# Performance work log

Measured on AMD Instinct MI355X. Metric: run time of the kernel, lower is better.

The kernel has to match this reference:

```python
import jax, jax.numpy as jnp
import numpy as np
import math

B, S, H = 2, 2048, 2048
NH, LD = 16, 512
HD = H // NH


def setup_inputs() -> dict:
    key = jax.random.key(0)
    ks = jax.random.split(key, 9)
    sc = 0.02
    return {
        "x": jax.random.normal(ks[0], (B, S, H), dtype=jnp.float32),
        "wq": jax.random.normal(ks[1], (H, H), dtype=jnp.float32) * sc,
        "bq": jnp.zeros((H,), dtype=jnp.float32),
        "wk_lat": jax.random.normal(ks[2], (H, LD), dtype=jnp.float32) * sc,
        "wv_lat": jax.random.normal(ks[3], (H, LD), dtype=jnp.float32) * sc,
        "wk": jax.random.normal(ks[4], (LD, H), dtype=jnp.float32) * sc,
        "wv": jax.random.normal(ks[5], (LD, H), dtype=jnp.float32) * sc,
        "wo": jax.random.normal(ks[6], (H, H), dtype=jnp.float32) * sc,
        "bo": jnp.zeros((H,), dtype=jnp.float32),
    }


def reference(x, wq, bq, wk_lat, wv_lat, wk, wv, wo, bo):
    b, s, _ = x.shape
    # projections
    q = (x @ wq + bq).reshape(b, s, NH, HD).transpose(0, 2, 1, 3)  # [B,NH,S,HD]
    k_lat = x @ wk_lat  # [B,S,LD]
    v_lat = x @ wv_lat
    k = (k_lat @ wk).reshape(b, s, NH, HD).transpose(0, 2, 1, 3)
    v = (v_lat @ wv).reshape(b, s, NH, HD).transpose(0, 2, 1, 3)
    # causal attention
    scores = jnp.einsum('bhqd,bhkd->bhqk', q, k) / math.sqrt(HD)
    mask = jnp.tril(jnp.ones((s, s), dtype=bool))  # True = keep
    scores = jnp.where(mask, scores, -jnp.inf)
    weights = jax.nn.softmax(scores, axis=-1)
    out = jnp.einsum('bhqk,bhkd->bhqd', weights, v)
    out = out.transpose(0, 2, 1, 3).reshape(b, s, H)
    return out @ wo + bo
```

## Files before the change

kernel.cpp:

```cpp
#include <hip/hip_runtime.h>
#include <hip/hip_bf16.h>

#define PB   2
#define PS   2048
#define PH   2048
#define PNH  16
#define PLD  512
#define PHD  128
#define PM   (PB * PS)
#define PNCAT 3072
#define ATT_SCALE 0.08838834764831845f
#define ATT_MOFF 4.0f
#define ATT_SC2  0.12751744f
#define ATT_MO2  5.77078016f

typedef __attribute__((ext_vector_type(8))) short bf16x8;
typedef __attribute__((ext_vector_type(4))) float f32x4;

__device__ __forceinline__ unsigned short f2bf(float f) {
    unsigned int u = __float_as_uint(f);
    u += 0x7FFFu + ((u >> 16) & 1u);
    return (unsigned short)(u >> 16);
}

__device__ __forceinline__ void gl_lds16(const unsigned short* g, unsigned short* l) {
    __builtin_amdgcn_global_load_lds(
        (const __attribute__((address_space(1))) unsigned int*)g,
        (__attribute__((address_space(3))) unsigned int*)l, 16, 0, 0);
}

#define VMCNT(n)     asm volatile("s_waitcnt vmcnt(" #n ")" ::: "memory")
#define MEMFENCE()   asm volatile("" ::: "memory")

__global__ __launch_bounds__(256) void cast_f32_bf16_kernel(
    const float* __restrict__ in, unsigned short* __restrict__ out, int n)
{
    int i = (blockIdx.x * 256 + threadIdx.x) * 4;
    if (i >= n) return;
    float4 f = *(const float4*)(in + i);
    unsigned int a = (unsigned int)f2bf(f.x) | ((unsigned int)f2bf(f.y) << 16);
    unsigned int b = (unsigned int)f2bf(f.z) | ((unsigned int)f2bf(f.w) << 16);
    *(uint2*)(out + i) = make_uint2(a, b);
}

struct TC6 {
    const float* src[6];
    unsigned short* dst[6];
    int R[6];
    int C[6];
};

__global__ __launch_bounds__(256) void transpose_cast6_kernel(TC6 p)
{
    __shared__ float tile[32][33];
    const int z = blockIdx.z;
    const int r0 = blockIdx.y * 32, c0 = blockIdx.x * 32;
    const int R = p.R[z], C = p.C[z];
    if (r0 >= R || c0 >= C) return;
    const float* in = p.src[z];
    unsigned short* out = p.dst[z];
    int tx = threadIdx.x, ty = threadIdx.y;
#pragma unroll
    for (int i = 0; i < 32; i += 8)
        tile[ty + i][tx] = in[(size_t)(r0 + ty + i) * C + (c0 + tx)];
    __syncthreads();
#pragma unroll
    for (int i = 0; i < 32; i += 8)
        out[(size_t)(c0 + ty + i) * R + (r0 + tx)] = f2bf(tile[tx][ty + i]);
}

template<int EPI, bool HAS_BIAS>
__global__ __launch_bounds__(256, 3) void gemm97_kernel(
    const unsigned short* __restrict__ A, int lda,
    const unsigned short* __restrict__ BT,
    const float* __restrict__ bias, int nbias,
    void* __restrict__ Cout, int ldc, int K)
{
    __shared__ __align__(16) unsigned short As[128 * 64];
    __shared__ __align__(16) unsigned short Bs[128 * 64];

    const int tid  = threadIdx.x;
    const int wave = tid >> 6, lane = tid & 63;
    const int wm = wave >> 1, wn = wave & 1;
    const int quad = lane >> 4, l15 = lane & 15;
    const int sw = l15 & 7;

    const int gx  = gridDim.x;
    const int nwg = gx * gridDim.y;
    int wg = blockIdx.y * gx + blockIdx.x;
    if (!(nwg & 7)) wg = (wg & 7) * (nwg >> 3) + (wg >> 3);
    const int bm = (wg / gx) * 128, bn = (wg % gx) * 128;

    const int nt = K >> 6;

    const int srow = tid >> 3;
    const int scol = ((tid & 7) ^ (srow & 7)) << 3;
    const unsigned short* Ag = A  + (size_t)(bm + srow) * lda + scol;
    const unsigned short* Bg = BT + (size_t)(bn + srow) * K   + scol;
    unsigned short* const ldsA = &As[wave * 512];
    unsigned short* const ldsB = &Bs[wave * 512];

    auto ldA = [&](int m, int ks) -> bf16x8 {
        int ra = wm * 64 + m * 16 + l15;
        return *(const bf16x8*)&As[ra * 64 + (((ks * 4 + quad) ^ sw) << 3)];
    };
    auto ldB = [&](int j, int ks) -> bf16x8 {
        int rb = wn * 64 + j * 16 + l15;
        return *(const bf16x8*)&Bs[rb * 64 + (((ks * 4 + quad) ^ sw) << 3)];
    };

    f32x4 acc[4][4] = {};

    for (int kt = 0; kt < nt; ++kt) {
        const int k0 = kt * 64;
#pragma unroll
        for (int s = 0; s < 4; ++s) {
            gl_lds16(Ag + (size_t)(s * 32) * lda + k0, ldsA + s * 2048);
            gl_lds16(Bg + (size_t)(s * 32) * K   + k0, ldsB + s * 2048);
        }
        VMCNT(0);
        __syncthreads();

        bf16x8 bfr[4][2];
#pragma unroll
        for (int j = 0; j < 4; ++j)
#pragma unroll
            for (int ks = 0; ks < 2; ++ks) bfr[j][ks] = ldB(j, ks);
#pragma unroll
        for (int m = 0; m < 4; ++m) {
            bf16x8 a0 = ldA(m, 0), a1 = ldA(m, 1);
#pragma unroll
            for (int j = 0; j < 4; ++j) {
                acc[m][j] = __builtin_amdgcn_mfma_f32_16x16x32_bf16(a0, bfr[j][0], acc[m][j], 0, 0, 0);
                acc[m][j] = __builtin_amdgcn_mfma_f32_16x16x32_bf16(a1, bfr[j][1], acc[m][j], 0, 0, 0);
            }
        }
        __syncthreads();
    }

#pragma unroll
    for (int m = 0; m < 4; ++m)
#pragma unroll
        for (int j = 0; j < 4; ++j)
#pragma unroll
            for (int r = 0; r < 4; ++r) {
                int row = bm + wm * 64 + m * 16 + quad * 4 + r;
                int col = bn + wn * 64 + j * 16 + l15;
                float val = acc[m][j][r];
                if (HAS_BIAS && col < nbias) val += bias[col];
                if (EPI == 2) {
                    int bb = row >> 11, s = row & 2047, hh = col >> 7, d = col & 127;
                    size_t idx = ((size_t)((bb << 4) + hh) << 18) + ((size_t)(s >> 6) << 13)
                               + ((d >> 3) << 9) + ((s & 63) << 3) + (d & 7);
                    ((unsigned short*)Cout)[idx] = f2bf(val);
                } else if (EPI == 3) {
                    int bb = row >> 11, s = row & 2047, hh = col >> 7, d = col & 127;
                    size_t idx = ((size_t)((bb << 4) + hh) << 18) + ((size_t)(s >> 6) << 13)
                               + (((s >> 3) & 7) << 10) + (d << 3) + (s & 7);
                    ((unsigned short*)Cout)[idx] = f2bf(val);
                } else if (EPI == 1) {
                    ((float*)Cout)[(size_t)row * ldc + col] = val;
                } else {
                    ((unsigned short*)Cout)[(size_t)row * ldc + col] = f2bf(val);
                }
            }
}

__global__ __launch_bounds__(256, 3) void flash_attn_mfma_kernel(
    const unsigned short* __restrict__ q,
    const unsigned short* __restrict__ kswz,
    const unsigned short* __restrict__ vswz,
    unsigned short* __restrict__ o)
{
    __shared__ __align__(16) unsigned short Kl[8192];
    __shared__ __align__(16) unsigned short Vl[8192];
    __shared__ __align__(16) unsigned short Ps[4][16][76];

    const int tid  = threadIdx.x;
    const int wave = tid >> 6;
    const int lane = tid & 63;
    const int quad = lane >> 4, l15 = lane & 15;

    const int bid = blockIdx.x;
    const int qt = 31 - (bid >> 5);
    const int bh = bid & 31;
    const int b  = bh >> 4, h = bh & 15;
    const int q0 = qt * 64;

    const unsigned short* qbase = q + (size_t)(b * PS + q0) * PNCAT + h * PHD;
    const unsigned short* kbase = kswz + ((size_t)bh << 18);
    const unsigned short* vbase = vswz + ((size_t)bh << 18);

    auto stageK = [&](int it) {
        const unsigned short* kt = kbase + ((size_t)it << 13);
#pragma unroll
        for (int j = 0; j < 4; ++j)
            gl_lds16(kt + (wave * 4 + j) * 512 + lane * 8, &Kl[(wave * 4 + j) * 512]);
    };
    auto stageV = [&](int it) {
        const unsigned short* vt = vbase + ((size_t)it << 13);
#pragma unroll
        for (int j = 0; j < 4; ++j)
            gl_lds16(vt + (wave * 4 + j) * 512 + lane * 8, &Vl[(wave * 4 + j) * 512]);
    };

    bf16x8 aq[4];
#pragma unroll
    for (int kk = 0; kk < 4; ++kk)
        aq[kk] = *(const bf16x8*)(qbase + (size_t)(wave * 16 + l15) * PNCAT + kk * 32 + quad * 8);

    bf16x8 vones;
#pragma unroll
    for (int j = 0; j < 8; ++j) vones[j] = (short)0x3F80;

    f32x4 oacc[8] = {};
    f32x4 lacc = {};

    for (int it = 0; it <= qt; ++it) {
        __syncthreads();
        stageK(it);
        stageV(it);
        VMCNT(4);
        __builtin_amdgcn_s_barrier();
        MEMFENCE();

        f32x4 sacc[4] = {};
#pragma unroll
        for (int kk = 0; kk < 4; ++kk)
#pragma unroll
            for (int n = 0; n < 4; ++n) {
                bf16x8 bk = *(const bf16x8*)&Kl[((kk * 4 + quad) * 64 + n * 16 + l15) * 8];
                sacc[n] = __builtin_amdgcn_mfma_f32_16x16x32_bf16(aq[kk], bk, sacc[n], 0, 0, 0);
            }

        const bool diag = (it == qt);
#pragma unroll
        for (int n = 0; n < 4; ++n)
#pragma unroll
            for (int r = 0; r < 4; ++r) {
                float p = exp2f(fmaf(sacc[n][r], ATT_SC2, -ATT_MO2));
                if (diag && (n * 16 + l15 > wave * 16 + quad * 4 + r)) p = 0.0f;
                Ps[wave][quad * 4 + r][n * 16 + l15] = f2bf(p);
            }

        __syncthreads();

#pragma unroll
        for (int kk = 0; kk < 2; ++kk) {
            bf16x8 ap = *(const bf16x8*)&Ps[wave][l15][kk * 32 + quad * 8];
            lacc = __builtin_amdgcn_mfma_f32_16x16x32_bf16(ap, vones, lacc, 0, 0, 0);
#pragma unroll
            for (int n = 0; n < 8; ++n) {
                bf16x8 bv = *(const bf16x8*)&Vl[((kk * 4 + quad) * 128 + n * 16 + l15) * 8];
                oacc[n] = __builtin_amdgcn_mfma_f32_16x16x32_bf16(ap, bv, oacc[n], 0, 0, 0);
            }
        }
    }

    float inv[4];
#pragma unroll
    for (int r = 0; r < 4; ++r) inv[r] = 1.0f / lacc[r];
#pragma unroll
    for (int n = 0; n < 8; ++n)
#pragma unroll
        for (int r = 0; r < 4; ++r) {
            int row = q0 + wave * 16 + quad * 4 + r;
            int col = h * PHD + n * 16 + l15;
            o[(size_t)(b * PS + row) * PH + col] = f2bf(oacc[n][r] * inv[r]);
        }
}

extern "C" void kernel_launch(void* const* d_in, const int* in_sizes, int n_in,
                              void* d_out, int out_size, void* d_ws, size_t ws_size,
                              hipStream_t stream)
{
    const float* x      = (const float*)d_in[0];
    const float* wq     = (const float*)d_in[1];
    const float* bq     = (const float*)d_in[2];
    const float* wk_lat = (const float*)d_in[3];
    const float* wv_lat = (const float*)d_in[4];
    const float* wk     = (const float*)d_in[5];
    const float* wv     = (const float*)d_in[6];
    const float* wo     = (const float*)d_in[7];
    const float* bo     = (const float*)d_in[8];
    float* out = (float*)d_out;

    char* ws = (char*)d_ws;
    size_t off = 0;
    auto alloc = [&](size_t bytes) -> void* {
        void* p = ws + off;
        off += (bytes + 255) & ~(size_t)255;
        return p;
    };
    unsigned short* xb    = (unsigned short*)alloc((size_t)PM * PH * 2);
    unsigned short* wcatT = (unsigned short*)alloc((size_t)PNCAT * PH * 2);
    unsigned short* wkT   = (unsigned short*)alloc((size_t)PH * PLD * 2);
    unsigned short* wvT   = (unsigned short*)alloc((size_t)PH * PLD * 2);
    unsigned short* woT   = (unsigned short*)alloc((size_t)PH * PH * 2);
    unsigned short* cat   = (unsigned short*)alloc((size_t)PM * PNCAT * 2);
    unsigned short* kswz  = (unsigned short*)alloc((size_t)PM * PH * 2);
    unsigned short* attn  = (unsigned short*)alloc((size_t)PM * PH * 2);
    unsigned short* vswz  = xb;

    unsigned short* wqT    = wcatT;
    unsigned short* wkLatT = wcatT + (size_t)PH * PH;
    unsigned short* wvLatT = wcatT + (size_t)(PH + PLD) * PH;

    cast_f32_bf16_kernel<<<(PM * PH) / 4 / 256, 256, 0, stream>>>(x, xb, PM * PH);

    TC6 tc;
    tc.src[0] = wq;     tc.dst[0] = wqT;    tc.R[0] = PH;  tc.C[0] = PH;
    tc.src[1] = wk_lat; tc.dst[1] = wkLatT; tc.R[1] = PH;  tc.C[1] = PLD;
    tc.src[2] = wv_lat; tc.dst[2] = wvLatT; tc.R[2] = PH;  tc.C[2] = PLD;
    tc.src[3] = wk;     tc.dst[3] = wkT;    tc.R[3] = PLD; tc.C[3] = PH;
    tc.src[4] = wv;     tc.dst[4] = wvT;    tc.R[4] = PLD; tc.C[4] = PH;
    tc.src[5] = wo;     tc.dst[5] = woT;    tc.R[5] = PH;  tc.C[5] = PH;
    transpose_cast6_kernel<<<dim3(64, 64, 6), dim3(32, 8), 0, stream>>>(tc);

    gemm97_kernel<0, true><<<dim3(PNCAT / 128, PM / 128), 256, 0, stream>>>(
        xb, PH, wcatT, bq, PH, cat, PNCAT, PH);

    gemm97_kernel<2, false><<<dim3(PH / 128, PM / 128), 256, 0, stream>>>(
        cat + PH, PNCAT, wkT, nullptr, 0, kswz, 0, PLD);
    gemm97_kernel<3, false><<<dim3(PH / 128, PM / 128), 256, 0, stream>>>(
        cat + PH + PLD, PNCAT, wvT, nullptr, 0, vswz, 0, PLD);

    flash_attn_mfma_kernel<<<PB * PNH * (PS / 64), 256, 0, stream>>>(cat, kswz, vswz, attn);

    gemm97_kernel<1, true><<<dim3(PH / 128, PM / 128), 256, 0, stream>>>(
        attn, PH, woT, bo, PH, out, PH, PH);
}
```

Measured before the change: 337.1 us.

## Rewrite flash attention with 32x32 MFMA, 128-row query tiles and S^T formulation

The attention kernel now processes 128 query rows per block (32 per wave) instead of 64, switching from 16x16x32 to 32x32x16 bf16 MFMA and computing S^T = K·Q so each lane owns one query row. Row sums are accumulated in registers instead of through an extra ones-MFMA, and P is packed with v_cvt_pk_bf16. The K swizzle layout in the GEMM epilogue changes to match the new fragment reads. Halving the grid roughly doubles the K/V reuse per block, but it leaves fewer blocks and a coarser causal tail, and it raises register pressure from the 16-wide accumulators.

```diff
diff --git a/kernel.cpp b/kernel.cpp
--- a/kernel.cpp
+++ b/kernel.cpp
@@ -16,6 +16,7 @@
 
 typedef __attribute__((ext_vector_type(8))) short bf16x8;
 typedef __attribute__((ext_vector_type(4))) float f32x4;
+typedef __attribute__((ext_vector_type(16))) float f32x16;
 
 __device__ __forceinline__ unsigned short f2bf(float f) {
     unsigned int u = __float_as_uint(f);
@@ -31,6 +32,12 @@
 
 #define VMCNT(n)     asm volatile("s_waitcnt vmcnt(" #n ")" ::: "memory")
 #define MEMFENCE()   asm volatile("" ::: "memory")
+
+__device__ __forceinline__ unsigned int cvtpk_bf16(float lo, float hi) {
+    unsigned int r;
+    asm("v_cvt_pk_bf16_f32 %0, %1, %2" : "=v"(r) : "v"(lo), "v"(hi));
+    return r;
+}
 
 __global__ __launch_bounds__(256) void cast_f32_bf16_kernel(
     const float* __restrict__ in, unsigned short* __restrict__ out, int n)
@@ -151,7 +158,7 @@
                 if (EPI == 2) {
                     int bb = row >> 11, s = row & 2047, hh = col >> 7, d = col & 127;
                     size_t idx = ((size_t)((bb << 4) + hh) << 18) + ((size_t)(s >> 6) << 13)
-                               + ((d >> 3) << 9) + ((s & 63) << 3) + (d & 7);
+                               + ((d >> 4) << 10) + (((d >> 3) & 1) << 9) + ((s & 63) << 3) + (d & 7);
                     ((unsigned short*)Cout)[idx] = f2bf(val);
                 } else if (EPI == 3) {
                     int bb = row >> 11, s = row & 2047, hh = col >> 7, d = col & 127;
@@ -174,20 +181,21 @@
 {
     __shared__ __align__(16) unsigned short Kl[8192];
     __shared__ __align__(16) unsigned short Vl[8192];
-    __shared__ __align__(16) unsigned short Ps[4][16][76];
+    __shared__ __align__(16) unsigned short Pl[4][32][68];
 
     const int tid  = threadIdx.x;
     const int wave = tid >> 6;
     const int lane = tid & 63;
-    const int quad = lane >> 4, l15 = lane & 15;
+    const int l31 = lane & 31, hf = lane >> 5;
 
     const int bid = blockIdx.x;
-    const int qt = 31 - (bid >> 5);
+    const int qt = 15 - (bid >> 5);
     const int bh = bid & 31;
     const int b  = bh >> 4, h = bh & 15;
-    const int q0 = qt * 64;
-
-    const unsigned short* qbase = q + (size_t)(b * PS + q0) * PNCAT + h * PHD;
+    const int q0 = qt * 128;
+    const int nt = 2 * (qt + 1);
+
+    const unsigned short* qbase = q + (size_t)(b * PS + q0 + wave * 32 + l31) * PNCAT + h * PHD;
     const unsigned short* kbase = kswz + ((size_t)bh << 18);
     const unsigned short* vbase = vswz + ((size_t)bh << 18);
 
@@ -204,19 +212,16 @@
             gl_lds16(vt + (wave * 4 + j) * 512 + lane * 8, &Vl[(wave * 4 + j) * 512]);
     };
 
-    bf16x8 aq[4];
-#pragma unroll
-    for (int kk = 0; kk < 4; ++kk)
-        aq[kk] = *(const bf16x8*)(qbase + (size_t)(wave * 16 + l15) * PNCAT + kk * 32 + quad * 8);
-
-    bf16x8 vones;
-#pragma unroll
-    for (int j = 0; j < 8; ++j) vones[j] = (short)0x3F80;
-
-    f32x4 oacc[8] = {};
-    f32x4 lacc = {};
-
-    for (int it = 0; it <= qt; ++it) {
+    bf16x8 qf[8];
+#pragma unroll
+    for (int kk = 0; kk < 8; ++kk)
+        qf[kk] = *(const bf16x8*)(qbase + kk * 16 + hf * 8);
+
+    const int qrow = q0 + wave * 32 + l31;
+    f32x16 oacc[4] = {};
+    float lsum = 0.0f;
+
+    for (int it = 0; it < nt; ++it) {
         __syncthreads();
         stageK(it);
         stageV(it);
@@ -224,50 +229,63 @@
         __builtin_amdgcn_s_barrier();
         MEMFENCE();
 
-        f32x4 sacc[4] = {};
-#pragma unroll
-        for (int kk = 0; kk < 4; ++kk)
-#pragma unroll
-            for (int n = 0; n < 4; ++n) {
-                bf16x8 bk = *(const bf16x8*)&Kl[((kk * 4 + quad) * 64 + n * 16 + l15) * 8];
-                sacc[n] = __builtin_amdgcn_mfma_f32_16x16x32_bf16(aq[kk], bk, sacc[n], 0, 0, 0);
-            }
-
-        const bool diag = (it == qt);
-#pragma unroll
-        for (int n = 0; n < 4; ++n)
-#pragma unroll
-            for (int r = 0; r < 4; ++r) {
-                float p = exp2f(fmaf(sacc[n][r], ATT_SC2, -ATT_MO2));
-                if (diag && (n * 16 + l15 > wave * 16 + quad * 4 + r)) p = 0.0f;
-                Ps[wave][quad * 4 + r][n * 16 + l15] = f2bf(p);
-            }
+#pragma unroll
+        for (int m32 = 0; m32 < 2; ++m32) {
+            f32x16 s = {};
+#pragma unroll
+            for (int kk = 0; kk < 8; ++kk) {
+                bf16x8 ak = *(const bf16x8*)&Kl[(((kk * 2 + hf) * 64) + m32 * 32 + l31) * 8];
+                s = __builtin_amdgcn_mfma_f32_32x32x16_bf16(ak, qf[kk], s, 0, 0, 0);
+            }
+            const int kbase0 = it * 64 + m32 * 32 + 4 * hf;
+            const bool needmask = (it * 64 + m32 * 32 + 31) > (q0 + wave * 32);
+#pragma unroll
+            for (int r = 0; r < 16; r += 2) {
+                float p0 = exp2f(fmaf(s[r],     ATT_SC2, -ATT_MO2));
+                float p1 = exp2f(fmaf(s[r + 1], ATT_SC2, -ATT_MO2));
+                if (needmask) {
+                    int key = kbase0 + (r & 3) + 8 * (r >> 2);
+                    p0 = (key     <= qrow) ? p0 : 0.0f;
+                    p1 = (key + 1 <= qrow) ? p1 : 0.0f;
+                }
+                lsum += p0 + p1;
+                *(unsigned int*)&Pl[wave][l31][m32 * 32 + 4 * hf + 8 * (r >> 2) + (r & 3)]
+                    = cvtpk_bf16(p0, p1);
+            }
+        }
+
+        bf16x8 pa[4];
+#pragma unroll
+        for (int ks = 0; ks < 4; ++ks) {
+            uint2 w0 = *(const uint2*)&Pl[wave][l31][ks * 16 + hf * 8];
+            uint2 w1 = *(const uint2*)&Pl[wave][l31][ks * 16 + hf * 8 + 4];
+            uint4 w = {w0.x, w0.y, w1.x, w1.y};
+            pa[ks] = *(bf16x8*)&w;
+        }
 
         __syncthreads();
 
 #pragma unroll
-        for (int kk = 0; kk < 2; ++kk) {
-            bf16x8 ap = *(const bf16x8*)&Ps[wave][l15][kk * 32 + quad * 8];
-            lacc = __builtin_amdgcn_mfma_f32_16x16x32_bf16(ap, vones, lacc, 0, 0, 0);
-#pragma unroll
-            for (int n = 0; n < 8; ++n) {
-                bf16x8 bv = *(const bf16x8*)&Vl[((kk * 4 + quad) * 128 + n * 16 + l15) * 8];
-                oacc[n] = __builtin_amdgcn_mfma_f32_16x16x32_bf16(ap, bv, oacc[n], 0, 0, 0);
-            }
-        }
+        for (int ks = 0; ks < 4; ++ks)
+#pragma unroll
+            for (int dg = 0; dg < 4; ++dg) {
+                bf16x8 bv = *(const bf16x8*)&Vl[(((ks * 2 + hf) * 128) + dg * 32 + l31) * 8];
+                oacc[dg] = __builtin_amdgcn_mfma_f32_32x32x16_bf16(pa[ks], bv, oacc[dg], 0, 0, 0);
+            }
     }
 
-    float inv[4];
-#pragma unroll
-    for (int r = 0; r < 4; ++r) inv[r] = 1.0f / lacc[r];
-#pragma unroll
-    for (int n = 0; n < 8; ++n)
-#pragma unroll
-        for (int r = 0; r < 4; ++r) {
-            int row = q0 + wave * 16 + quad * 4 + r;
-            int col = h * PHD + n * 16 + l15;
-            o[(size_t)(b * PS + row) * PH + col] = f2bf(oacc[n][r] * inv[r]);
-        }
+    const float ltot = lsum + __shfl_xor(lsum, 32);
+    const float inv = 1.0f / ltot;
+
+#pragma unroll
+    for (int r = 0; r < 16; ++r) {
+        const int ql = (r & 3) + 8 * (r >> 2) + 4 * hf;
+        const float sc = __shfl(inv, ql, 32);
+        const size_t grow = (size_t)(b * PS + q0 + wave * 32 + ql) * PH + h * PHD;
+#pragma unroll
+        for (int dg = 0; dg < 4; ++dg)
+            o[grow + dg * 32 + l31] = f2bf(oacc[dg][r] * sc);
+    }
 }
 
 extern "C" void kernel_launch(void* const* d_in, const int* in_sizes, int n_in,
@@ -325,7 +343,7 @@
     gemm97_kernel<3, false><<<dim3(PH / 128, PM / 128), 256, 0, stream>>>(
         cat + PH + PLD, PNCAT, wvT, nullptr, 0, vswz, 0, PLD);
 
-    flash_attn_mfma_kernel<<<PB * PNH * (PS / 64), 256, 0, stream>>>(cat, kswz, vswz, attn);
+    flash_attn_mfma_kernel<<<PB * PNH * (PS / 128), 256, 0, stream>>>(cat, kswz, vswz, attn);
 
     gemm97_kernel<1, true><<<dim3(PH / 128, PM / 128), 256, 0, stream>>>(
         attn, PH, woT, bo, PH, out, PH, PH);
```

Measured after the change: 357.9 us. 1.06x slower.
